# Optimization experiments

Hardware: AMD Instinct MI355X
Metric: run time of the kernel (lower is better)

Reference implementation:

```python
import jax, jax.numpy as jnp
import numpy as np
from jax import lax

# Faithful JAX translation of Laplacian_Forward_Model.forward(acc=False).
# The opaque approximate multiplier (mul_wrapper) is modeled as an exact
# multiply, under which approx_sharp and accurate_sharp produce identical
# values; the original assigns x.data = approx result (values) while grads
# flow through the accurate path, so with exact multiply the single accurate
# path (with straight-through floor) reproduces the full forward math.

LAPLACIAN = np.array([-1.0, -1.0, -1.0, -1.0, 8.0, -1.0, -1.0, -1.0, -1.0]) / 8.0


def setup_inputs() -> dict:
    key = jax.random.key(0)
    k_in, = jax.random.split(key, 1)
    B = 16384
    n_mult = 1  # len(mul_approx_func_arr)
    inp = jax.random.uniform(k_in, (B, 1, 32, 32), dtype=jnp.float32) * 255.0
    weight = jnp.asarray(np.tile(LAPLACIAN, (n_mult, 1)), dtype=jnp.float32)          # (n_mult, 9)
    weight_factor = jnp.asarray(np.tile(np.array([8.0]), (n_mult, 1)), dtype=jnp.float32)  # (n_mult, 1)
    return {"input": inp, "weight": weight, "weight_factor": weight_factor}


def _sharp(x, ker):
    # depthwise 3x3 conv, padding 1 (C=1 so plain conv)
    B = x.shape[0]
    conv = lax.conv_general_dilated(x, ker, window_strides=(1, 1),
                                    padding=((1, 1), (1, 1)),
                                    dimension_numbers=("NCHW", "OIHW", "NCHW"))
    flat = conv.reshape(B, -1)
    cmax = lax.stop_gradient(flat.max(axis=1)).reshape(B, 1, 1, 1)
    cmin = lax.stop_gradient(flat.min(axis=1)).reshape(B, 1, 1, 1)
    mod = (conv - cmin) / jnp.maximum(cmax - cmin, 1e-6) * 255.0
    sharpened = x + mod
    sflat = sharpened.reshape(B, -1)
    smax = lax.stop_gradient(sflat.max(axis=1)).reshape(B, 1, 1, 1)
    smin = lax.stop_gradient(sflat.min(axis=1)).reshape(B, 1, 1, 1)
    res = jnp.clip((sharpened - smin) / jnp.clip(smax - smin, 1e-6, 255.0) * 255.0, 0.0, 255.0)
    # result.data = floor(result.data): straight-through floor
    return res + lax.stop_gradient(jnp.floor(res) - res)


def reference(input, weight, weight_factor):
    n_mult = weight.shape[0]
    outs = []
    for ii in range(n_mult):  # small fixed loop over approx-multiplier variants
        wc = jnp.clip(weight[ii], -0.999, 0.999)            # clamp + hardtanh(-1,1)
        wf = jnp.clip(weight_factor[ii], 1.001, 254.999)    # clamp + hardtanh(1,255)
        ker = (wc * wf).reshape(1, 1, 3, 3).astype(input.dtype)
        outs.append(_sharp(input, ker))
    return jnp.stack(outs, 0)  # (n_mult, B, 1, 32, 32)
```

## Files before the change

kernel.cpp:

```cpp
#include <hip/hip_runtime.h>
#include <math.h>


#define S 40

template <int CTRL>
__device__ __forceinline__ float dppmov(float x) {
    return __int_as_float(__builtin_amdgcn_update_dpp(
        __float_as_int(x), __float_as_int(x), CTRL, 0xf, 0xf, false));
}

__device__ __forceinline__ void wave64_minmax(float& mn, float& mx) {
    mn = fminf(mn, dppmov<0x111>(mn)); mx = fmaxf(mx, dppmov<0x111>(mx));
    mn = fminf(mn, dppmov<0x112>(mn)); mx = fmaxf(mx, dppmov<0x112>(mx));
    mn = fminf(mn, dppmov<0x114>(mn)); mx = fmaxf(mx, dppmov<0x114>(mx));
    mn = fminf(mn, dppmov<0x118>(mn)); mx = fmaxf(mx, dppmov<0x118>(mx));
    mn = fminf(mn, dppmov<0x142>(mn)); mx = fmaxf(mx, dppmov<0x142>(mx));
    mn = fminf(mn, dppmov<0x143>(mn)); mx = fmaxf(mx, dppmov<0x143>(mx));
}

__global__ __launch_bounds__(256) void laplacian_fwd_kernel(
    const float* __restrict__ in,
    const float* __restrict__ weight,
    const float* __restrict__ wfac,
    float* __restrict__ out)
{
    __shared__ float img[34 * S];
    __shared__ __align__(16) float redA[8];
    __shared__ __align__(16) float redB[8];

    const int b = blockIdx.x;
    const int t = threadIdx.x;
    const float* src = in + (size_t)b * 1024;
    float* dst = out + (size_t)b * 1024;

    const int row  = t >> 3;
    const int col0 = (t & 7) << 2;

    const float4 x4 = *(const float4*)(src + row * 32 + col0);

    if (t < 40)       img[t] = 0.0f;
    else if (t < 80)  img[33 * S + (t - 40)] = 0.0f;
    else if (t < 112) img[(t - 79) * S + 3]  = 0.0f;
    else if (t < 144) img[(t - 111) * S + 36] = 0.0f;

    const float wf = fminf(fmaxf(wfac[0], 1.001f), 254.999f);
    float k[9];
#pragma unroll
    for (int i = 0; i < 9; ++i)
        k[i] = fminf(fmaxf(weight[i], -0.999f), 0.999f) * wf;

    *(float4*)&img[(row + 1) * S + (col0 + 4)] = x4;
    __syncthreads();

    const float* pt = &img[ row      * S + col0];
    const float* pm = &img[(row + 1) * S + col0];
    const float* pb = &img[(row + 2) * S + col0];
    const float  tl = pt[3], tr = pt[8];
    const float4 tm = *(const float4*)(pt + 4);
    const float  ml = pm[3], mr = pm[8];
    const float  bl = pb[3], br = pb[8];
    const float4 bm = *(const float4*)(pb + 4);

    float conv[4];
    conv[0] = k[0]*tl   + k[1]*tm.x + k[2]*tm.y
            + k[3]*ml   + k[4]*x4.x + k[5]*x4.y
            + k[6]*bl   + k[7]*bm.x + k[8]*bm.y;
    conv[1] = k[0]*tm.x + k[1]*tm.y + k[2]*tm.z
            + k[3]*x4.x + k[4]*x4.y + k[5]*x4.z
            + k[6]*bm.x + k[7]*bm.y + k[8]*bm.z;
    conv[2] = k[0]*tm.y + k[1]*tm.z + k[2]*tm.w
            + k[3]*x4.y + k[4]*x4.z + k[5]*x4.w
            + k[6]*bm.y + k[7]*bm.z + k[8]*bm.w;
    conv[3] = k[0]*tm.z + k[1]*tm.w + k[2]*tr
            + k[3]*x4.z + k[4]*x4.w + k[5]*mr
            + k[6]*bm.z + k[7]*bm.w + k[8]*br;

    const int wv = t >> 6;

    float mn = fminf(fminf(conv[0], conv[1]), fminf(conv[2], conv[3]));
    float mx = fmaxf(fmaxf(conv[0], conv[1]), fmaxf(conv[2], conv[3]));
    wave64_minmax(mn, mx);
    if ((t & 63) == 63) { redA[wv] = mn; redA[4 + wv] = mx; }
    __syncthreads();
    const float4 amn = *(const float4*)&redA[0];
    const float4 amx = *(const float4*)&redA[4];
    const float cmin = fminf(fminf(amn.x, amn.y), fminf(amn.z, amn.w));
    const float cmax = fmaxf(fmaxf(amx.x, amx.y), fmaxf(amx.z, amx.w));

    const float inv1 = 255.0f / fmaxf(cmax - cmin, 1e-6f);
    const float xv[4] = {x4.x, x4.y, x4.z, x4.w};
    float sh[4];
#pragma unroll
    for (int j = 0; j < 4; ++j)
        sh[j] = xv[j] + (conv[j] - cmin) * inv1;

    mn = fminf(fminf(sh[0], sh[1]), fminf(sh[2], sh[3]));
    mx = fmaxf(fmaxf(sh[0], sh[1]), fmaxf(sh[2], sh[3]));
    wave64_minmax(mn, mx);
    if ((t & 63) == 63) { redB[wv] = mn; redB[4 + wv] = mx; }
    __syncthreads();
    const float4 bmn = *(const float4*)&redB[0];
    const float4 bmx = *(const float4*)&redB[4];
    const float smin = fminf(fminf(bmn.x, bmn.y), fminf(bmn.z, bmn.w));
    const float smax = fmaxf(fmaxf(bmx.x, bmx.y), fmaxf(bmx.z, bmx.w));

    const float inv2 = 255.0f / fminf(fmaxf(smax - smin, 1e-6f), 255.0f);
    float4 o;
    o.x = floorf(fminf(fmaxf((sh[0] - smin) * inv2, 0.0f), 255.0f));
    o.y = floorf(fminf(fmaxf((sh[1] - smin) * inv2, 0.0f), 255.0f));
    o.z = floorf(fminf(fmaxf((sh[2] - smin) * inv2, 0.0f), 255.0f));
    o.w = floorf(fminf(fmaxf((sh[3] - smin) * inv2, 0.0f), 255.0f));
    *(float4*)(dst + row * 32 + col0) = o;
}

extern "C" void kernel_launch(void* const* d_in, const int* in_sizes, int n_in,
                              void* d_out, int out_size, void* d_ws, size_t ws_size,
                              hipStream_t stream) {
    const float* in   = (const float*)d_in[0];
    const float* w    = (const float*)d_in[1];
    const float* wfac = (const float*)d_in[2];
    float* out = (float*)d_out;
    const int B = in_sizes[0] / 1024;
    laplacian_fwd_kernel<<<B, 256, 0, stream>>>(in, w, wfac, out);
}
```

Before: 118.0 us.

## Process each image with a single wavefront, replacing LDS reductions with readlane

Each block shrinks from 256 threads to one 64-lane wavefront, and every thread now handles four rows of four pixels. Because one wavefront covers the whole image, the two cross-wave min/max reductions through shared memory, and their barriers, are replaced by DPP reductions plus readlane. This removes two block barriers and the LDS reduction traffic. In exchange there are fewer threads per block and more registers per thread, which could hurt latency hiding. The cmin expression has a redundant conditional that evaluates to the same value on both branches.

```diff
diff --git a/kernel.cpp b/kernel.cpp
--- a/kernel.cpp
+++ b/kernel.cpp
@@ -19,30 +19,29 @@
     mn = fminf(mn, dppmov<0x143>(mn)); mx = fmaxf(mx, dppmov<0x143>(mx));
 }
 
-__global__ __launch_bounds__(256) void laplacian_fwd_kernel(
+__global__ __launch_bounds__(64) void laplacian_fwd_kernel(
     const float* __restrict__ in,
     const float* __restrict__ weight,
     const float* __restrict__ wfac,
     float* __restrict__ out)
 {
     __shared__ float img[34 * S];
-    __shared__ __align__(16) float redA[8];
-    __shared__ __align__(16) float redB[8];
 
     const int b = blockIdx.x;
     const int t = threadIdx.x;
     const float* src = in + (size_t)b * 1024;
     float* dst = out + (size_t)b * 1024;
 
-    const int row  = t >> 3;
-    const int col0 = (t & 7) << 2;
+    const int rbase = t >> 3;
+    const int col0  = (t & 7) << 2;
 
-    const float4 x4 = *(const float4*)(src + row * 32 + col0);
+    float4 x4[4];
+#pragma unroll
+    for (int i = 0; i < 4; ++i)
+        x4[i] = *(const float4*)(src + i * 256 + t * 4);
 
-    if (t < 40)       img[t] = 0.0f;
-    else if (t < 80)  img[33 * S + (t - 40)] = 0.0f;
-    else if (t < 112) img[(t - 79) * S + 3]  = 0.0f;
-    else if (t < 144) img[(t - 111) * S + 36] = 0.0f;
+    if (t < 40) { img[t] = 0.0f; img[33 * S + t] = 0.0f; }
+    if (t < 32) { img[(t + 1) * S + 3] = 0.0f; img[(t + 1) * S + 36] = 0.0f; }
 
     const float wf = fminf(fmaxf(wfac[0], 1.001f), 254.999f);
     float k[9];
@@ -50,68 +49,84 @@
     for (int i = 0; i < 9; ++i)
         k[i] = fminf(fmaxf(weight[i], -0.999f), 0.999f) * wf;
 
-    *(float4*)&img[(row + 1) * S + (col0 + 4)] = x4;
+#pragma unroll
+    for (int i = 0; i < 4; ++i)
+        *(float4*)&img[(i * 8 + rbase + 1) * S + (col0 + 4)] = x4[i];
     __syncthreads();
 
-    const float* pt = &img[ row      * S + col0];
-    const float* pm = &img[(row + 1) * S + col0];
-    const float* pb = &img[(row + 2) * S + col0];
-    const float  tl = pt[3], tr = pt[8];
-    const float4 tm = *(const float4*)(pt + 4);
-    const float  ml = pm[3], mr = pm[8];
-    const float  bl = pb[3], br = pb[8];
-    const float4 bm = *(const float4*)(pb + 4);
+    float conv[4][4];
+#pragma unroll
+    for (int i = 0; i < 4; ++i) {
+        const int row = i * 8 + rbase;
+        const float* pt = &img[ row      * S + col0];
+        const float* pm = &img[(row + 1) * S + col0];
+        const float* pb = &img[(row + 2) * S + col0];
+        const float  tl = pt[3], tr = pt[8];
+        const float4 tm = *(const float4*)(pt + 4);
+        const float  ml = pm[3], mr = pm[8];
+        const float  bl = pb[3], br = pb[8];
+        const float4 bm = *(const float4*)(pb + 4);
+        const float4 m  = x4[i];
+        conv[i][0] = k[0]*tl   + k[1]*tm.x + k[2]*tm.y
+                   + k[3]*ml   + k[4]*m.x  + k[5]*m.y
+                   + k[6]*bl   + k[7]*bm.x + k[8]*bm.y;
+        conv[i][1] = k[0]*tm.x + k[1]*tm.y + k[2]*tm.z
+                   + k[3]*m.x  + k[4]*m.y  + k[5]*m.z
+                   + k[6]*bm.x + k[7]*bm.y + k[8]*bm.z;
+        conv[i][2] = k[0]*tm.y + k[1]*tm.z + k[2]*tm.w
+                   + k[3]*m.y  + k[4]*m.z  + k[5]*m.w
+                   + k[6]*bm.y + k[7]*bm.z + k[8]*bm.w;
+        conv[i][3] = k[0]*tm.z + k[1]*tm.w + k[2]*tr
+                   + k[3]*m.z  + k[4]*m.w  + k[5]*mr
+                   + k[6]*bm.z + k[7]*bm.w + k[8]*br;
+    }
 
-    float conv[4];
-    conv[0] = k[0]*tl   + k[1]*tm.x + k[2]*tm.y
-            + k[3]*ml   + k[4]*x4.x + k[5]*x4.y
-            + k[6]*bl   + k[7]*bm.x + k[8]*bm.y;
-    conv[1] = k[0]*tm.x + k[1]*tm.y + k[2]*tm.z
-            + k[3]*x4.x + k[4]*x4.y + k[5]*x4.z
-            + k[6]*bm.x + k[7]*bm.y + k[8]*bm.z;
-    conv[2] = k[0]*tm.y + k[1]*tm.z + k[2]*tm.w
-            + k[3]*x4.y + k[4]*x4.z + k[5]*x4.w
-            + k[6]*bm.y + k[7]*bm.z + k[8]*bm.w;
-    conv[3] = k[0]*tm.z + k[1]*tm.w + k[2]*tr
-            + k[3]*x4.z + k[4]*x4.w + k[5]*mr
-            + k[6]*bm.z + k[7]*bm.w + k[8]*br;
-
-    const int wv = t >> 6;
-
-    float mn = fminf(fminf(conv[0], conv[1]), fminf(conv[2], conv[3]));
-    float mx = fmaxf(fmaxf(conv[0], conv[1]), fmaxf(conv[2], conv[3]));
+    float mn = conv[0][0], mx = conv[0][0];
+#pragma unroll
+    for (int i = 0; i < 4; ++i)
+#pragma unroll
+        for (int j = 0; j < 4; ++j) {
+            mn = fminf(mn, conv[i][j]);
+            mx = fmaxf(mx, conv[i][j]);
+        }
     wave64_minmax(mn, mx);
-    if ((t & 63) == 63) { redA[wv] = mn; redA[4 + wv] = mx; }
-    __syncthreads();
-    const float4 amn = *(const float4*)&redA[0];
-    const float4 amx = *(const float4*)&redA[4];
-    const float cmin = fminf(fminf(amn.x, amn.y), fminf(amn.z, amn.w));
-    const float cmax = fmaxf(fmaxf(amx.x, amx.y), fmaxf(amx.z, amx.w));
+    const float cmin = __builtin_amdgcn_readlane(__float_as_int(mn), 63) == 0
+                       ? __int_as_float(__builtin_amdgcn_readlane(__float_as_int(mn), 63))
+                       : __int_as_float(__builtin_amdgcn_readlane(__float_as_int(mn), 63));
+    const float cmax = __int_as_float(__builtin_amdgcn_readlane(__float_as_int(mx), 63));
 
     const float inv1 = 255.0f / fmaxf(cmax - cmin, 1e-6f);
-    const float xv[4] = {x4.x, x4.y, x4.z, x4.w};
-    float sh[4];
+    float sh[4][4];
 #pragma unroll
-    for (int j = 0; j < 4; ++j)
-        sh[j] = xv[j] + (conv[j] - cmin) * inv1;
+    for (int i = 0; i < 4; ++i) {
+        sh[i][0] = x4[i].x + (conv[i][0] - cmin) * inv1;
+        sh[i][1] = x4[i].y + (conv[i][1] - cmin) * inv1;
+        sh[i][2] = x4[i].z + (conv[i][2] - cmin) * inv1;
+        sh[i][3] = x4[i].w + (conv[i][3] - cmin) * inv1;
+    }
 
-    mn = fminf(fminf(sh[0], sh[1]), fminf(sh[2], sh[3]));
-    mx = fmaxf(fmaxf(sh[0], sh[1]), fmaxf(sh[2], sh[3]));
+    mn = sh[0][0]; mx = sh[0][0];
+#pragma unroll
+    for (int i = 0; i < 4; ++i)
+#pragma unroll
+        for (int j = 0; j < 4; ++j) {
+            mn = fminf(mn, sh[i][j]);
+            mx = fmaxf(mx, sh[i][j]);
+        }
     wave64_minmax(mn, mx);
-    if ((t & 63) == 63) { redB[wv] = mn; redB[4 + wv] = mx; }
-    __syncthreads();
-    const float4 bmn = *(const float4*)&redB[0];
-    const float4 bmx = *(const float4*)&redB[4];
-    const float smin = fminf(fminf(bmn.x, bmn.y), fminf(bmn.z, bmn.w));
-    const float smax = fmaxf(fmaxf(bmx.x, bmx.y), fmaxf(bmx.z, bmx.w));
+    const float smin = __int_as_float(__builtin_amdgcn_readlane(__float_as_int(mn), 63));
+    const float smax = __int_as_float(__builtin_amdgcn_readlane(__float_as_int(mx), 63));
 
     const float inv2 = 255.0f / fminf(fmaxf(smax - smin, 1e-6f), 255.0f);
-    float4 o;
-    o.x = floorf(fminf(fmaxf((sh[0] - smin) * inv2, 0.0f), 255.0f));
-    o.y = floorf(fminf(fmaxf((sh[1] - smin) * inv2, 0.0f), 255.0f));
-    o.z = floorf(fminf(fmaxf((sh[2] - smin) * inv2, 0.0f), 255.0f));
-    o.w = floorf(fminf(fmaxf((sh[3] - smin) * inv2, 0.0f), 255.0f));
-    *(float4*)(dst + row * 32 + col0) = o;
+#pragma unroll
+    for (int i = 0; i < 4; ++i) {
+        float4 o;
+        o.x = floorf(fminf(fmaxf((sh[i][0] - smin) * inv2, 0.0f), 255.0f));
+        o.y = floorf(fminf(fmaxf((sh[i][1] - smin) * inv2, 0.0f), 255.0f));
+        o.z = floorf(fminf(fmaxf((sh[i][2] - smin) * inv2, 0.0f), 255.0f));
+        o.w = floorf(fminf(fmaxf((sh[i][3] - smin) * inv2, 0.0f), 255.0f));
+        *(float4*)(dst + i * 256 + t * 4) = o;
+    }
 }
 
 extern "C" void kernel_launch(void* const* d_in, const int* in_sizes, int n_in,
@@ -122,5 +137,5 @@
     const float* wfac = (const float*)d_in[2];
     float* out = (float*)d_out;
     const int B = in_sizes[0] / 1024;
-    laplacian_fwd_kernel<<<B, 256, 0, stream>>>(in, w, wfac, out);
+    laplacian_fwd_kernel<<<B, 64, 0, stream>>>(in, w, wfac, out);
 }
```

After: 112.0 us. 5.1% less time.
